# Performance work log

Hardware: AMD Instinct MI355X
Metric: run time of the kernel (lower is better)

Reference implementation:

```python
import jax, jax.numpy as jnp
import numpy as np

N = 4096        # nodes
E = 131072      # edges (avg degree 32)
IN = 256        # in_channels
OUT = 64        # out_channels per head
HEADS = 4


def setup_inputs() -> dict:
    key = jax.random.key(0)
    k1, k2, k3, k4 = jax.random.split(key, 4)
    h = jax.random.normal(k1, (N, IN), dtype=jnp.float32)
    edge_index = jax.random.randint(k2, (2, E), 0, N, dtype=jnp.int64)
    # Linear weights, one per head: [HEADS, OUT, IN] (torch Linear layout)
    W = jax.random.normal(k3, (HEADS, OUT, IN), dtype=jnp.float32) * (1.0 / np.sqrt(IN))
    # attention vector a: xavier_uniform with gain=1.414, shape [2*OUT, 1]
    limit = 1.414 * np.sqrt(6.0 / (2 * OUT + 1))
    a = jax.random.uniform(k4, (HEADS, 2 * OUT, 1), dtype=jnp.float32, minval=-limit, maxval=limit)
    return {"h": h, "edge_index": edge_index, "W": W, "a": a}


def _head(h, row, col, Wf, af):
    # Wh = Linear(h): [N, OUT]
    Wh = h @ Wf.T
    # e = leakyrelu(cat(Wh[row], Wh[col]) @ a) == Wh[row]@a1 + Wh[col]@a2
    a1 = af[:OUT, 0]
    a2 = af[OUT:, 0]
    e = jax.nn.leaky_relu(Wh[row] @ a1 + Wh[col] @ a2, negative_slope=0.2)
    # dense N x N scatter (faithful to original: non-edges contribute exp(0))
    alpha = jnp.zeros((h.shape[0], h.shape[0]), dtype=h.dtype).at[row, col].set(e)
    alpha = jax.nn.softmax(alpha, axis=1)
    h_prime = alpha @ Wh  # [N, OUT]
    return h_prime, alpha


def reference(h, edge_index, W, a):
    row, col = edge_index[0], edge_index[1]
    # vmap over heads: h_prime [HEADS, N, OUT], attn [HEADS, N, N]
    h_prime, attn = jax.vmap(lambda Wf, af: _head(h, row, col, Wf, af))(W, a)
    # concat heads along features, then relu
    out = jax.nn.relu(jnp.transpose(h_prime, (1, 0, 2)).reshape(h.shape[0], HEADS * OUT))
    return out, attn.mean(axis=0)
```

## Files before the change

kernel.cpp:

```cpp
#include <hip/hip_runtime.h>

#define N_NODES 4096
#define E_EDGES 131072
#define IN_F    256
#define OUT_F   64
#define HEADS   4
#define HC      256
#define CAP     128

typedef float v4f __attribute__((ext_vector_type(4)));
typedef short v8s __attribute__((ext_vector_type(8)));
typedef float v4acc __attribute__((ext_vector_type(4)));

__device__ __forceinline__ unsigned short bf16_rn(float x) {
    unsigned u = __builtin_bit_cast(unsigned, x);
    unsigned r = (u + 0x7FFFu + ((u >> 16) & 1u)) >> 16;
    return (unsigned short)r;
}
__device__ __forceinline__ float bf16_to_f(unsigned short b) {
    unsigned u = ((unsigned)b) << 16;
    return __builtin_bit_cast(float, u);
}

__global__ void k_init_prep(const float* __restrict__ h, const float* __restrict__ W,
                            unsigned short* __restrict__ h_hi, unsigned short* __restrict__ h_lo,
                            unsigned short* __restrict__ W_hi, unsigned short* __restrict__ W_lo,
                            int* __restrict__ rowcnt, float* __restrict__ S) {
    const int i = blockIdx.x * blockDim.x + threadIdx.x;
    if (i < N_NODES) rowcnt[i] = 0;
    if (i < HC)      S[i] = 0.f;
    const int HN = N_NODES * IN_F;
    const int WN = HC * IN_F;
    if (i < HN) {
        float x = h[i];
        unsigned short hi = bf16_rn(x);
        h_hi[i] = hi;
        h_lo[i] = bf16_rn(x - bf16_to_f(hi));
    } else if (i < HN + WN) {
        int j = i - HN;
        float x = W[j];
        unsigned short hi = bf16_rn(x);
        W_hi[j] = hi;
        W_lo[j] = bf16_rn(x - bf16_to_f(hi));
    }
}

__global__ __launch_bounds__(256) void k_linear_mfma(
        const unsigned short* __restrict__ h_hi, const unsigned short* __restrict__ h_lo,
        const unsigned short* __restrict__ W_hi, const unsigned short* __restrict__ W_lo,
        const float* __restrict__ a,
        float* __restrict__ Wh, float* __restrict__ s1, float* __restrict__ s2,
        float* __restrict__ S) {
    const int t = threadIdx.x;
    const int wave = t >> 6, lane = t & 63;
    const int n16 = lane & 15, quad = lane >> 4;
    const int node0 = blockIdx.x * 16;
    const int ch0 = wave * 64;
    const int head = wave;

    v4acc acc[4];
#pragma unroll
    for (int nt = 0; nt < 4; ++nt) acc[nt] = (v4acc){0.f, 0.f, 0.f, 0.f};

    const int arow = (node0 + n16) * IN_F;
#pragma unroll
    for (int s = 0; s < 8; ++s) {
        const int k0 = s * 32 + quad * 8;
        v8s Ah = *(const v8s*)(h_hi + arow + k0);
        v8s Al = *(const v8s*)(h_lo + arow + k0);
#pragma unroll
        for (int nt = 0; nt < 4; ++nt) {
            const int ch = ch0 + nt * 16 + n16;
            v8s Bh = *(const v8s*)(W_hi + ch * IN_F + k0);
            v8s Bl = *(const v8s*)(W_lo + ch * IN_F + k0);
            acc[nt] = __builtin_amdgcn_mfma_f32_16x16x32_bf16(Ah, Bh, acc[nt], 0, 0, 0);
            acc[nt] = __builtin_amdgcn_mfma_f32_16x16x32_bf16(Ah, Bl, acc[nt], 0, 0, 0);
            acc[nt] = __builtin_amdgcn_mfma_f32_16x16x32_bf16(Al, Bh, acc[nt], 0, 0, 0);
        }
    }

#pragma unroll
    for (int nt = 0; nt < 4; ++nt) {
        const int ch = ch0 + nt * 16 + n16;
#pragma unroll
        for (int r = 0; r < 4; ++r)
            Wh[(size_t)(node0 + quad * 4 + r) * HC + ch] = acc[nt][r];
    }

    float a1v[4], a2v[4];
#pragma unroll
    for (int nt = 0; nt < 4; ++nt) {
        a1v[nt] = a[head * 2 * OUT_F + nt * 16 + n16];
        a2v[nt] = a[head * 2 * OUT_F + OUT_F + nt * 16 + n16];
    }
#pragma unroll
    for (int r = 0; r < 4; ++r) {
        float p1 = acc[0][r] * a1v[0] + acc[1][r] * a1v[1] + acc[2][r] * a1v[2] + acc[3][r] * a1v[3];
        float p2 = acc[0][r] * a2v[0] + acc[1][r] * a2v[1] + acc[2][r] * a2v[2] + acc[3][r] * a2v[3];
#pragma unroll
        for (int o = 1; o < 16; o <<= 1) {
            p1 += __shfl_xor(p1, o, 64);
            p2 += __shfl_xor(p2, o, 64);
        }
        if (n16 == 0) {
            const int node = node0 + quad * 4 + r;
            s1[node * HEADS + head] = p1;
            s2[node * HEADS + head] = p2;
        }
    }

#pragma unroll
    for (int nt = 0; nt < 4; ++nt) {
        float cp = acc[nt][0] + acc[nt][1] + acc[nt][2] + acc[nt][3];
        cp += __shfl_xor(cp, 16, 64);
        cp += __shfl_xor(cp, 32, 64);
        if (quad == 0) atomicAdd(&S[ch0 + nt * 16 + n16], cp);
    }
}

__global__ void k_append(const int* __restrict__ rows, int* __restrict__ rowcnt,
                         int* __restrict__ slots) {
    const int k = blockIdx.x * blockDim.x + threadIdx.x;
    const int r = rows[k];
    const int pos = atomicAdd(&rowcnt[r], 1);
    if (pos < CAP) slots[r * CAP + pos] = k;
}

__global__ __launch_bounds__(256) void k_stats(
        const int* __restrict__ rowcnt, const int* __restrict__ slots,
        const int* __restrict__ cols,
        const float* __restrict__ s1, const float* __restrict__ s2,
        const float* __restrict__ S, const float* __restrict__ Wh,
        float* __restrict__ out0, float* __restrict__ bsum,
        int* __restrict__ gnw, int* __restrict__ gcol, float* __restrict__ gws) {
    __shared__ float eh[HEADS][CAP];
    __shared__ int   kk[CAP];
    __shared__ int   cc[CAP];
    __shared__ int   wcol[CAP];
    __shared__ float weh[HEADS][CAP];
    __shared__ float wgt[HEADS][CAP];
    __shared__ float mh[HEADS], dh[HEADS], bh[HEADS];
    __shared__ int   nw_sh;

    const int i = blockIdx.x;
    const int t = threadIdx.x, head = t >> 6, lane = t & 63;
    int cnt = rowcnt[i];
    if (cnt > CAP) cnt = CAP;
    if (t == 0) nw_sh = 0;

    const float4 s1r = *(const float4*)(s1 + i * HEADS);

    for (int q = t; q < cnt; q += 256) {
        const int k = slots[i * CAP + q];
        const int c = cols[k];
        kk[q] = k; cc[q] = c;
        const float4 s2c = *(const float4*)(s2 + c * HEADS);
        float x;
        x = s1r.x + s2c.x; eh[0][q] = (x > 0.f) ? x : 0.2f * x;
        x = s1r.y + s2c.y; eh[1][q] = (x > 0.f) ? x : 0.2f * x;
        x = s1r.z + s2c.z; eh[2][q] = (x > 0.f) ? x : 0.2f * x;
        x = s1r.w + s2c.w; eh[3][q] = (x > 0.f) ? x : 0.2f * x;
    }
    __syncthreads();

    for (int q = t; q < cnt; q += 256) {
        const int c = cc[q], k = kk[q];
        int win = 1;
        for (int q2 = 0; q2 < cnt; ++q2)
            if (cc[q2] == c && kk[q2] > k) { win = 0; break; }
        if (win) {
            const int pos = atomicAdd(&nw_sh, 1);
            wcol[pos] = c;
            weh[0][pos] = eh[0][q]; weh[1][pos] = eh[1][q];
            weh[2][pos] = eh[2][q]; weh[3][pos] = eh[3][q];
        }
    }
    __syncthreads();
    const int nw = nw_sh;

    float emax = -1e30f;
    for (int q = lane; q < nw; q += 64) emax = fmaxf(emax, weh[head][q]);
#pragma unroll
    for (int o = 32; o > 0; o >>= 1) emax = fmaxf(emax, __shfl_xor(emax, o, 64));
    const float m = fmaxf(emax, 0.f);

    float ssum = 0.f;
    for (int q = lane; q < nw; q += 64) ssum += __expf(weh[head][q] - m);
#pragma unroll
    for (int o = 32; o > 0; o >>= 1) ssum += __shfl_xor(ssum, o, 64);

    if (lane == 0) {
        const float denom = ssum + (float)(N_NODES - nw) * __expf(-m);
        mh[head] = m;
        dh[head] = denom;
        bh[head] = __expf(-m) / denom;
    }
    __syncthreads();

    for (int q = t; q < nw; q += 256) {
        const float w0 = __expf(weh[0][q] - mh[0]) / dh[0];
        const float w1 = __expf(weh[1][q] - mh[1]) / dh[1];
        const float w2 = __expf(weh[2][q] - mh[2]) / dh[2];
        const float w3 = __expf(weh[3][q] - mh[3]) / dh[3];
        wgt[0][q] = w0; wgt[1][q] = w1; wgt[2][q] = w2; wgt[3][q] = w3;
        gcol[i * CAP + q] = wcol[q];
        gws[i * CAP + q]  = 0.25f * (w0 + w1 + w2 + w3);
    }
    if (t == 0) {
        gnw[i] = nw;
        bsum[i] = 0.25f * (bh[0] + bh[1] + bh[2] + bh[3]);
    }
    __syncthreads();

    const float b_ = bh[head];
    float acc = b_ * S[t];
    for (int q = 0; q < nw; ++q)
        acc += (wgt[head][q] - b_) * Wh[(size_t)wcol[q] * HC + t];
    out0[(size_t)i * HC + t] = fmaxf(acc, 0.f);
}

__global__ __launch_bounds__(256) void k_attn_fill(const float* __restrict__ bsum,
                                                   float* __restrict__ attn) {
    const int i = blockIdx.x;
    const float v = bsum[i];
    const float4 v4 = make_float4(v, v, v, v);
    float4* rowp = (float4*)(attn + (size_t)i * N_NODES);
#pragma unroll
    for (int rep = 0; rep < 4; ++rep)
        rowp[rep * 256 + threadIdx.x] = v4;
}

__global__ __launch_bounds__(256) void k_attn_scatter(
        const int* __restrict__ gnw, const int* __restrict__ gcol,
        const float* __restrict__ gws, float* __restrict__ attn) {
    const int wave = threadIdx.x >> 6, lane = threadIdx.x & 63;
    const int i = blockIdx.x * 4 + wave;
    const int nw = gnw[i];
    for (int q = lane; q < nw; q += 64)
        attn[(size_t)i * N_NODES + gcol[i * CAP + q]] = gws[i * CAP + q];
}

extern "C" void kernel_launch(void* const* d_in, const int* in_sizes, int n_in,
                              void* d_out, int out_size, void* d_ws, size_t ws_size,
                              hipStream_t stream) {
    const float* h  = (const float*)d_in[0];
    const int*   ei = (const int*)d_in[1];
    const float* W  = (const float*)d_in[2];
    const float* a  = (const float*)d_in[3];
    const int* rows = ei;
    const int* cols = ei + E_EDGES;

    float* out0 = (float*)d_out;
    float* attn = out0 + (size_t)N_NODES * HC;

    char* p = (char*)d_ws;
    auto carve = [&](size_t bytes) { char* q = p; p += (bytes + 255) & ~(size_t)255; return q; };
    float* Wh      = (float*)carve(sizeof(float) * (size_t)N_NODES * HC);
    float* s1      = (float*)carve(sizeof(float) * N_NODES * HEADS);
    float* s2      = (float*)carve(sizeof(float) * N_NODES * HEADS);
    float* S       = (float*)carve(sizeof(float) * HC);
    float* bsum    = (float*)carve(sizeof(float) * N_NODES);
    int*   rowcnt  = (int*)carve(sizeof(int) * N_NODES);
    int*   slots   = (int*)carve(sizeof(int) * (size_t)N_NODES * CAP);
    int*   gnw     = (int*)carve(sizeof(int) * N_NODES);
    int*   gcol    = (int*)carve(sizeof(int) * (size_t)N_NODES * CAP);
    float* gws     = (float*)carve(sizeof(float) * (size_t)N_NODES * CAP);
    unsigned short* h_hi = (unsigned short*)carve(sizeof(short) * (size_t)N_NODES * IN_F);
    unsigned short* h_lo = (unsigned short*)carve(sizeof(short) * (size_t)N_NODES * IN_F);
    unsigned short* W_hi = (unsigned short*)carve(sizeof(short) * HC * IN_F);
    unsigned short* W_lo = (unsigned short*)carve(sizeof(short) * HC * IN_F);

    k_init_prep<<<(N_NODES * IN_F + HC * IN_F) / 256, 256, 0, stream>>>(
        h, W, h_hi, h_lo, W_hi, W_lo, rowcnt, S);
    k_linear_mfma<<<N_NODES / 16, 256, 0, stream>>>(h_hi, h_lo, W_hi, W_lo, a, Wh, s1, s2, S);
    k_append<<<E_EDGES / 256, 256, 0, stream>>>(rows, rowcnt, slots);
    k_stats<<<N_NODES, 256, 0, stream>>>(rowcnt, slots, cols, s1, s2, S, Wh,
                                         out0, bsum, gnw, gcol, gws);
    k_attn_fill<<<N_NODES, 256, 0, stream>>>(bsum, attn);
    k_attn_scatter<<<N_NODES / 4, 256, 0, stream>>>(gnw, gcol, gws, attn);
}
```

Before: 153.2 us.

## Fuse append into prep kernel and attn fill/scatter via LDS row buffer

Merges the edge-append pass into the bf16 split kernel as extra blocks, replacing the zero-init with a memset of a contiguous S+rowcnt region. Combines the dense attention fill and sparse scatter into one kernel that builds each row in shared memory and then streams it out. This removes kernel launches and the second scattered write pass over the large attention matrix. It costs 16KB of LDS per block, which may lower occupancy for the streaming write.

```diff
diff --git a/kernel.cpp b/kernel.cpp
--- a/kernel.cpp
+++ b/kernel.cpp
@@ -8,6 +8,9 @@
 #define HC      256
 #define CAP     128
 
+#define PREP_BLOCKS ((N_NODES * IN_F + HC * IN_F) / 256)
+#define APP_BLOCKS  (E_EDGES / 256)
+
 typedef float v4f __attribute__((ext_vector_type(4)));
 typedef short v8s __attribute__((ext_vector_type(8)));
 typedef float v4acc __attribute__((ext_vector_type(4)));
@@ -22,26 +25,32 @@
     return __builtin_bit_cast(float, u);
 }
 
-__global__ void k_init_prep(const float* __restrict__ h, const float* __restrict__ W,
-                            unsigned short* __restrict__ h_hi, unsigned short* __restrict__ h_lo,
-                            unsigned short* __restrict__ W_hi, unsigned short* __restrict__ W_lo,
-                            int* __restrict__ rowcnt, float* __restrict__ S) {
-    const int i = blockIdx.x * blockDim.x + threadIdx.x;
-    if (i < N_NODES) rowcnt[i] = 0;
-    if (i < HC)      S[i] = 0.f;
-    const int HN = N_NODES * IN_F;
-    const int WN = HC * IN_F;
-    if (i < HN) {
-        float x = h[i];
-        unsigned short hi = bf16_rn(x);
-        h_hi[i] = hi;
-        h_lo[i] = bf16_rn(x - bf16_to_f(hi));
-    } else if (i < HN + WN) {
-        int j = i - HN;
-        float x = W[j];
-        unsigned short hi = bf16_rn(x);
-        W_hi[j] = hi;
-        W_lo[j] = bf16_rn(x - bf16_to_f(hi));
+__global__ void k_prep_append(const float* __restrict__ h, const float* __restrict__ W,
+                              unsigned short* __restrict__ h_hi, unsigned short* __restrict__ h_lo,
+                              unsigned short* __restrict__ W_hi, unsigned short* __restrict__ W_lo,
+                              const int* __restrict__ rows,
+                              int* __restrict__ rowcnt, int* __restrict__ slots) {
+    const int b = blockIdx.x;
+    if (b < PREP_BLOCKS) {
+        const int i = b * 256 + threadIdx.x;
+        const int HN = N_NODES * IN_F;
+        if (i < HN) {
+            float x = h[i];
+            unsigned short hi = bf16_rn(x);
+            h_hi[i] = hi;
+            h_lo[i] = bf16_rn(x - bf16_to_f(hi));
+        } else {
+            int j = i - HN;
+            float x = W[j];
+            unsigned short hi = bf16_rn(x);
+            W_hi[j] = hi;
+            W_lo[j] = bf16_rn(x - bf16_to_f(hi));
+        }
+    } else {
+        const int k = (b - PREP_BLOCKS) * 256 + threadIdx.x;
+        const int r = rows[k];
+        const int pos = atomicAdd(&rowcnt[r], 1);
+        if (pos < CAP) slots[r * CAP + pos] = k;
     }
 }
 
@@ -116,14 +125,6 @@
         cp += __shfl_xor(cp, 32, 64);
         if (quad == 0) atomicAdd(&S[ch0 + nt * 16 + n16], cp);
     }
-}
-
-__global__ void k_append(const int* __restrict__ rows, int* __restrict__ rowcnt,
-                         int* __restrict__ slots) {
-    const int k = blockIdx.x * blockDim.x + threadIdx.x;
-    const int r = rows[k];
-    const int pos = atomicAdd(&rowcnt[r], 1);
-    if (pos < CAP) slots[r * CAP + pos] = k;
 }
 
 __global__ __launch_bounds__(256) void k_stats(
@@ -219,25 +220,26 @@
     out0[(size_t)i * HC + t] = fmaxf(acc, 0.f);
 }
 
-__global__ __launch_bounds__(256) void k_attn_fill(const float* __restrict__ bsum,
-                                                   float* __restrict__ attn) {
-    const int i = blockIdx.x;
+__global__ __launch_bounds__(256) void k_attn(
+        const float* __restrict__ bsum, const int* __restrict__ gnw,
+        const int* __restrict__ gcol, const float* __restrict__ gws,
+        float* __restrict__ attn) {
+    __shared__ float rowbuf[N_NODES];
+    const int i = blockIdx.x, t = threadIdx.x;
     const float v = bsum[i];
+    const int nw = gnw[i];
     const float4 v4 = make_float4(v, v, v, v);
-    float4* rowp = (float4*)(attn + (size_t)i * N_NODES);
+    float4* rb4 = (float4*)rowbuf;
+#pragma unroll
+    for (int rep = 0; rep < 4; ++rep) rb4[rep * 256 + t] = v4;
+    __syncthreads();
+    for (int q = t; q < nw; q += 256) rowbuf[gcol[i * CAP + q]] = gws[i * CAP + q];
+    __syncthreads();
+    const float4* src = (const float4*)rowbuf;
+    float4* dst = (float4*)(attn + (size_t)i * N_NODES);
 #pragma unroll
     for (int rep = 0; rep < 4; ++rep)
-        rowp[rep * 256 + threadIdx.x] = v4;
-}
-
-__global__ __launch_bounds__(256) void k_attn_scatter(
-        const int* __restrict__ gnw, const int* __restrict__ gcol,
-        const float* __restrict__ gws, float* __restrict__ attn) {
-    const int wave = threadIdx.x >> 6, lane = threadIdx.x & 63;
-    const int i = blockIdx.x * 4 + wave;
-    const int nw = gnw[i];
-    for (int q = lane; q < nw; q += 64)
-        attn[(size_t)i * N_NODES + gcol[i * CAP + q]] = gws[i * CAP + q];
+        dst[rep * 256 + t] = src[rep * 256 + t];
 }
 
 extern "C" void kernel_launch(void* const* d_in, const int* in_sizes, int n_in,
@@ -255,12 +257,12 @@
 
     char* p = (char*)d_ws;
     auto carve = [&](size_t bytes) { char* q = p; p += (bytes + 255) & ~(size_t)255; return q; };
+    float* S       = (float*)carve(sizeof(float) * HC + sizeof(int) * N_NODES);
+    int*   rowcnt  = (int*)(S + HC);
     float* Wh      = (float*)carve(sizeof(float) * (size_t)N_NODES * HC);
     float* s1      = (float*)carve(sizeof(float) * N_NODES * HEADS);
     float* s2      = (float*)carve(sizeof(float) * N_NODES * HEADS);
-    float* S       = (float*)carve(sizeof(float) * HC);
     float* bsum    = (float*)carve(sizeof(float) * N_NODES);
-    int*   rowcnt  = (int*)carve(sizeof(int) * N_NODES);
     int*   slots   = (int*)carve(sizeof(int) * (size_t)N_NODES * CAP);
     int*   gnw     = (int*)carve(sizeof(int) * N_NODES);
     int*   gcol    = (int*)carve(sizeof(int) * (size_t)N_NODES * CAP);
@@ -270,12 +272,11 @@
     unsigned short* W_hi = (unsigned short*)carve(sizeof(short) * HC * IN_F);
     unsigned short* W_lo = (unsigned short*)carve(sizeof(short) * HC * IN_F);
 
-    k_init_prep<<<(N_NODES * IN_F + HC * IN_F) / 256, 256, 0, stream>>>(
-        h, W, h_hi, h_lo, W_hi, W_lo, rowcnt, S);
+    hipMemsetAsync(S, 0, sizeof(float) * HC + sizeof(int) * N_NODES, stream);
+    k_prep_append<<<PREP_BLOCKS + APP_BLOCKS, 256, 0, stream>>>(
+        h, W, h_hi, h_lo, W_hi, W_lo, rows, rowcnt, slots);
     k_linear_mfma<<<N_NODES / 16, 256, 0, stream>>>(h_hi, h_lo, W_hi, W_lo, a, Wh, s1, s2, S);
-    k_append<<<E_EDGES / 256, 256, 0, stream>>>(rows, rowcnt, slots);
     k_stats<<<N_NODES, 256, 0, stream>>>(rowcnt, slots, cols, s1, s2, S, Wh,
                                          out0, bsum, gnw, gcol, gws);
-    k_attn_fill<<<N_NODES, 256, 0, stream>>>(bsum, attn);
-    k_attn_scatter<<<N_NODES / 4, 256, 0, stream>>>(gnw, gcol, gws, attn);
-}
+    k_attn<<<N_NODES, 256, 0, stream>>>(bsum, gnw, gcol, gws, attn);
+}
```

Measured after the change: 148.9 us. 2.8% less time.
